# Performance work log

Hardware: AMD Instinct MI355X
Metric: run time of the kernel (lower is better)

The kernel has to match this reference:

```python
import jax, jax.numpy as jnp
import numpy as np

N_NODES = 50000
N_EDGES = 800000
HID = 64
OUT = 64
REL = 5


def setup_inputs() -> dict:
    key = jax.random.key(0)
    ks = jax.random.split(key, 9)
    s_in = 1.0 / np.sqrt(HID)
    return {
        "contagion_risk": jax.random.normal(ks[0], (N_NODES, HID), jnp.float32),
        "edge_weight": jax.random.uniform(ks[1], (N_EDGES,), jnp.float32),
        # torch Linear weights stored transposed as [in, out] so y = x @ W + b
        "W_in_w": jax.random.uniform(ks[2], (HID, HID), jnp.float32, -s_in, s_in),
        "W_in_b": jax.random.uniform(ks[3], (HID,), jnp.float32, -s_in, s_in),
        "W_rel": jax.random.uniform(ks[4], (REL, HID, HID), jnp.float32, -s_in, s_in),
        "W_out_w": jax.random.uniform(ks[5], (HID, OUT), jnp.float32, -s_in, s_in),
        "W_out_b": jax.random.uniform(ks[6], (OUT,), jnp.float32, -s_in, s_in),
        "edge_index": jax.random.randint(ks[7], (2, N_EDGES), 0, N_NODES, jnp.int64 if jax.config.jax_enable_x64 else jnp.int32),
        "edge_type": jax.random.randint(ks[8], (N_EDGES,), 0, REL, jnp.int32),
        "num_nodes": N_NODES,
    }


def _dan_forward(contagion_risk, W_in_w, W_in_b, W_rel, W_out_w, W_out_b,
                 edge_index, edge_type, num_nodes):
    row, col = edge_index[0], edge_index[1]  # dst, src
    x = contagion_risk @ W_in_w + W_in_b                       # [N, H]
    x_j = x[col]                                               # [E, H] gather

    # gcn_norm (no self loops, unit edge weights): deg over col
    ones = jnp.ones(col.shape[0], x.dtype)
    deg = jax.ops.segment_sum(ones, col, num_segments=num_nodes)
    dis = jnp.where(deg > 0, jax.lax.rsqrt(jnp.maximum(deg, 1.0)), 0.0)
    norm_w = (dis[row] * dis[col])[:, None]                    # [E, 1]
    msg_gcn = jax.ops.segment_sum(x_j * norm_w, row, num_segments=num_nodes)

    # per-relation masked GEMM (grouped GEMM over REL relation types)
    res = jnp.zeros_like(x_j)
    for i in range(W_rel.shape[0]):
        mask = (edge_type == i)[:, None]
        res = res + jnp.where(mask, x_j @ W_rel[i], 0.0)

    # segment softmax over destination-node groups (per feature channel)
    seg_max = jax.ops.segment_max(res, row, num_segments=num_nodes)
    e = jnp.exp(res - seg_max[row])
    seg_sum = jax.ops.segment_sum(e, row, num_segments=num_nodes)
    weig = e / (seg_sum[row] + 1e-16)

    msg = jax.ops.segment_sum(res * weig, row, num_segments=num_nodes)
    out = (msg_gcn + 0.5 * jax.nn.relu(msg)) @ W_out_w + W_out_b
    return out


def reference(contagion_risk, edge_weight, W_in_w, W_in_b, W_rel, W_out_w, W_out_b,
              edge_index, edge_type, num_nodes):
    # edge_weight is accepted by the original forward but never used
    return _dan_forward(contagion_risk, W_in_w, W_in_b, W_rel, W_out_w, W_out_b,
                        edge_index, edge_type, num_nodes)
```

## Files before the change

### kernel.cpp

```cpp
#include <hip/hip_runtime.h>
#include <hip/hip_bf16.h>

#define HID 64
#define REL 5
#define EPB 2048

typedef short bf16x8 __attribute__((ext_vector_type(8)));
typedef float f32x4 __attribute__((ext_vector_type(4)));

__device__ __forceinline__ float bf2f(unsigned short u) {
    return __uint_as_float(((unsigned)u) << 16);
}
__device__ __forceinline__ unsigned short f2bf(float f) {
    __hip_bfloat16 h = (__hip_bfloat16)f;
    return *(unsigned short*)&h;
}
__device__ __forceinline__ void dec_edge(const int* __restrict__ ei, int i64,
                                         int E, int e, int& r, int& c) {
    if (i64) { r = ei[2 * e]; c = ei[2 * (E + e)]; }
    else     { r = ei[e];     c = ei[E + e]; }
}

__global__ void k_detect(const unsigned short* __restrict__ wb,
                         const int* __restrict__ ei, int* flags) {
    int lane = threadIdx.x;
    bool big = (lane < 32) ? (fabsf(bf2f(wb[2 * lane])) > 0.26f) : false;
    unsigned long long b1 = __ballot(big);
    bool odd_nz = (ei[2 * lane + 1] != 0);
    unsigned long long b2 = __ballot(odd_nz);
    if (lane == 0) {
        flags[0] = (b1 != 0ull) ? 1 : 0;
        flags[1] = (b2 == 0ull) ? 1 : 0;
    }
}

__global__ void k_pack(const void* Win, const void* bin, const void* Wr,
                       const void* Wout, const void* bout,
                       unsigned short* __restrict__ Bpk,
                       float* __restrict__ binf, float* __restrict__ boutf,
                       const int* __restrict__ flags) {
    int f = flags[0];
    int gid = blockIdx.x * 256 + threadIdx.x;
    if (gid < 7 * 2 * 4 * 64) {
        int lane = gid & 63;
        int nt = (gid >> 6) & 3;
        int ks = (gid >> 8) & 1;
        int mat = gid >> 9;
        int q = lane >> 4, n = nt * 16 + (lane & 15);
#pragma unroll
        for (int j = 0; j < 8; j++) {
            int k = ks * 32 + q * 8 + j;
            int idx = k * 64 + n;
            float val;
            if (mat == 0)
                val = f ? ((const float*)Win)[idx] : bf2f(((const unsigned short*)Win)[idx]);
            else if (mat <= 5) {
                int ii = (mat - 1) * 4096 + idx;
                val = f ? ((const float*)Wr)[ii] : bf2f(((const unsigned short*)Wr)[ii]);
            } else
                val = f ? ((const float*)Wout)[idx] : bf2f(((const unsigned short*)Wout)[idx]);
            Bpk[(size_t)gid * 8 + j] = f2bf(val);
        }
    }
    if (gid < 64)
        binf[gid] = f ? ((const float*)bin)[gid] : bf2f(((const unsigned short*)bin)[gid]);
    else if (gid >= 64 && gid < 128) {
        int i = gid - 64;
        boutf[i] = f ? ((const float*)bout)[i] : bf2f(((const unsigned short*)bout)[i]);
    }
}

__global__ void k_p1a(const int* __restrict__ ei, const int* __restrict__ flags,
                      int* __restrict__ hist, int E, int NB, int nblk) {
    extern __shared__ int lh[];
    int tid = threadIdx.x, blk = blockIdx.x;
    for (int i = tid; i < 2 * NB; i += 256) lh[i] = 0;
    __syncthreads();
    int i64 = flags[1];
#pragma unroll
    for (int k = 0; k < EPB / 256; k++) {
        int e = blk * EPB + k * 256 + tid;
        if (e < E) {
            int r, c;
            dec_edge(ei, i64, E, e, r, c);
            atomicAdd(&lh[r >> 6], 1);
            atomicAdd(&lh[NB + (c >> 6)], 1);
        }
    }
    __syncthreads();
    size_t NBn = (size_t)NB * nblk;
    for (int i = tid; i < NB; i += 256) {
        hist[(size_t)i * nblk + blk] = lh[i];
        hist[NBn + (size_t)i * nblk + blk] = lh[NB + i];
    }
}

__global__ void s_blk(const int* __restrict__ v, int* __restrict__ bsum, int M) {
    __shared__ int red[256];
    int t = threadIdx.x;
    int i0 = blockIdx.x * 1024 + t * 4;
    int s = 0;
#pragma unroll
    for (int j = 0; j < 4; j++) { int i = i0 + j; if (i < M) s += v[i]; }
    red[t] = s;
    __syncthreads();
    for (int d = 128; d > 0; d >>= 1) {
        if (t < d) red[t] += red[t + d];
        __syncthreads();
    }
    if (t == 0) bsum[blockIdx.x] = red[0];
}

__global__ void s_top(int* __restrict__ bsum, int nsb) {
    __shared__ int v[1024];
    int t = threadIdx.x;
    for (int i = t; i < nsb; i += 256) v[i] = bsum[i];
    __syncthreads();
    if (t == 0) {
        int run = 0;
        for (int i = 0; i < nsb; i++) { int x = v[i]; v[i] = run; run += x; }
    }
    __syncthreads();
    for (int i = t; i < nsb; i += 256) bsum[i] = v[i];
}

__global__ void s_apply(int* __restrict__ v, const int* __restrict__ bsum, int M) {
    __shared__ int red[256];
    int t = threadIdx.x;
    int i0 = blockIdx.x * 1024 + t * 4;
    int x[4];
    int s = 0;
#pragma unroll
    for (int j = 0; j < 4; j++) {
        int i = i0 + j;
        x[j] = (i < M) ? v[i] : 0;
        s += x[j];
    }
    red[t] = s;
    __syncthreads();
    for (int d = 1; d < 256; d <<= 1) {
        int add = (t >= d) ? red[t - d] : 0;
        __syncthreads();
        red[t] += add;
        __syncthreads();
    }
    int run = bsum[blockIdx.x] + red[t] - s;
#pragma unroll
    for (int j = 0; j < 4; j++) {
        int i = i0 + j;
        if (i < M) { int tmp = x[j]; v[i] = run; run += tmp; }
    }
}

__global__ void k_p1c(const int* __restrict__ ei, const int* __restrict__ et,
                      const int* __restrict__ flags, const int* __restrict__ hist,
                      unsigned* __restrict__ rbuf, unsigned char* __restrict__ cb8,
                      int E, int NB, int nblk) {
    extern __shared__ int lh[];
    int tid = threadIdx.x, blk = blockIdx.x;
    for (int i = tid; i < 2 * NB; i += 256) lh[i] = 0;
    __syncthreads();
    int i64 = flags[1];
    size_t NBn = (size_t)NB * nblk;
#pragma unroll
    for (int k = 0; k < EPB / 256; k++) {
        int e = blk * EPB + k * 256 + tid;
        if (e < E) {
            int r, c;
            dec_edge(ei, i64, E, e, r, c);
            int t = et[e];
            int binR = r >> 6;
            int posR = hist[(size_t)binR * nblk + blk] + atomicAdd(&lh[binR], 1);
            rbuf[posR] = ((unsigned)(r & 63) << 26) | ((unsigned)t << 17) | (unsigned)c;
            int binC = c >> 6;
            int posC = hist[NBn + (size_t)binC * nblk + blk] - E + atomicAdd(&lh[NB + binC], 1);
            cb8[posC] = (unsigned char)(c & 63);
        }
    }
}

__global__ void k_p2r(const unsigned* __restrict__ rbuf, const int* __restrict__ hist,
                      int* __restrict__ off, unsigned* __restrict__ edata4,
                      int E, int N, int NB, int nblk) {
    __shared__ int lcnt[64], excl[64], lcnt2[64];
    int tid = threadIdx.x, bk = blockIdx.x;
    int bstart = hist[(size_t)bk * nblk];
    int bend = (bk + 1 < NB) ? hist[(size_t)(bk + 1) * nblk] : E;
    if (tid < 64) { lcnt[tid] = 0; lcnt2[tid] = 0; }
    __syncthreads();
    for (int e = bstart + tid; e < bend; e += 256)
        atomicAdd(&lcnt[rbuf[e] >> 26], 1);
    __syncthreads();
    if (tid == 0) {
        int run = 0;
        for (int j = 0; j < 64; j++) { excl[j] = run; run += lcnt[j]; }
    }
    __syncthreads();
    if (tid < 64) {
        int node = bk * 64 + tid;
        if (node < N) off[node] = bstart + excl[tid];
    }
    if (bk == 0 && tid == 0) off[N] = E;
    for (int e = bstart + tid; e < bend; e += 256) {
        unsigned rec = rbuf[e];
        int rl = rec >> 26;
        int t = (rec >> 17) & 7;
        int c = rec & 0x1FFFF;
        int pos = bstart + excl[rl] + atomicAdd(&lcnt2[rl], 1);
        edata4[pos] = (unsigned)c | ((unsigned)t << 20);
    }
}

__global__ void k_p2c(const unsigned char* __restrict__ cb8, const int* __restrict__ hist,
                      float* __restrict__ dis, int E, int N, int NB, int nblk) {
    __shared__ int lcnt[64];
    int tid = threadIdx.x, bk = blockIdx.x;
    size_t NBn = (size_t)NB * nblk;
    int cstart = hist[NBn + (size_t)bk * nblk] - E;
    int cend = (bk + 1 < NB) ? hist[NBn + (size_t)(bk + 1) * nblk] - E : E;
    if (tid < 64) lcnt[tid] = 0;
    __syncthreads();
    for (int e = cstart + tid; e < cend; e += 256)
        atomicAdd(&lcnt[cb8[e]], 1);
    __syncthreads();
    if (tid < 64) {
        int node = bk * 64 + tid;
        if (node < N) {
            int d = lcnt[tid];
            dis[node] = (d > 0) ? rsqrtf((float)d) : 0.f;
        }
    }
}

__device__ __forceinline__ bf16x8 load_a8(const void* A, int f, size_t base) {
    if (f) {
        const float* Af = (const float*)A + base;
        bf16x8 r;
#pragma unroll
        for (int j = 0; j < 8; j++) r[j] = (short)f2bf(Af[j]);
        return r;
    }
    return *(const bf16x8*)((const unsigned short*)A + base);
}

__global__ void __launch_bounds__(256)
k_xy(const void* __restrict__ A, const unsigned short* __restrict__ Bpk,
     const float* __restrict__ binf, const float* __restrict__ dis,
     unsigned short* __restrict__ Yb, const int* __restrict__ flags,
     int N, int Np) {
    __shared__ unsigned short Bs[6 * 2 * 4 * 64 * 8];
    __shared__ unsigned short Xs[64 * 64];
    __shared__ float bs[64];
    int tid = threadIdx.x;
    for (int i = tid; i < 6 * 2 * 4 * 64; i += 256)
        ((uint4*)Bs)[i] = ((const uint4*)Bpk)[i];
    if (tid < 64) bs[tid] = binf[tid];
    __syncthreads();

    int w = tid >> 6, lane = tid & 63;
    int q = lane >> 4, n16 = lane & 15;
    int mrow = w * 16 + n16;
    int f = flags[0];
    int arow = min(blockIdx.x * 64 + mrow, N - 1);
    bf16x8 a0 = load_a8(A, f, (size_t)arow * 64 + 8 * q);
    bf16x8 a1 = load_a8(A, f, (size_t)arow * 64 + 8 * q + 32);

    float disv[4];
#pragma unroll
    for (int r = 0; r < 4; r++) {
        int node = blockIdx.x * 64 + w * 16 + 4 * q + r;
        disv[r] = (node < N) ? dis[node] : 0.f;
    }

#pragma unroll
    for (int nt = 0; nt < 4; nt++) {
        f32x4 d = {0.f, 0.f, 0.f, 0.f};
        bf16x8 b0 = *(const bf16x8*)(Bs + (size_t)(((0 * 2 + 0) * 4 + nt) * 64 + lane) * 8);
        bf16x8 b1 = *(const bf16x8*)(Bs + (size_t)(((0 * 2 + 1) * 4 + nt) * 64 + lane) * 8);
        d = __builtin_amdgcn_mfma_f32_16x16x32_bf16(a0, b0, d, 0, 0, 0);
        d = __builtin_amdgcn_mfma_f32_16x16x32_bf16(a1, b1, d, 0, 0, 0);
        int col = nt * 16 + n16;
        float bb = bs[col];
#pragma unroll
        for (int r = 0; r < 4; r++) {
            int rowl = w * 16 + 4 * q + r;
            float xval = d[r] + bb;
            Xs[rowl * 64 + col] = f2bf(xval);
            int node = blockIdx.x * 64 + rowl;
            if (node < N) Yb[((size_t)5 * Np + node) * 64 + col] = f2bf(xval * disv[r]);
        }
    }
    bf16x8 a20 = *(const bf16x8*)(Xs + mrow * 64 + 8 * q);
    bf16x8 a21 = *(const bf16x8*)(Xs + mrow * 64 + 8 * q + 32);

    for (int rel = 0; rel < REL; rel++) {
        int mat = 1 + rel;
#pragma unroll
        for (int nt = 0; nt < 4; nt++) {
            f32x4 d = {0.f, 0.f, 0.f, 0.f};
            bf16x8 b0 = *(const bf16x8*)(Bs + (size_t)(((mat * 2 + 0) * 4 + nt) * 64 + lane) * 8);
            bf16x8 b1 = *(const bf16x8*)(Bs + (size_t)(((mat * 2 + 1) * 4 + nt) * 64 + lane) * 8);
            d = __builtin_amdgcn_mfma_f32_16x16x32_bf16(a20, b0, d, 0, 0, 0);
            d = __builtin_amdgcn_mfma_f32_16x16x32_bf16(a21, b1, d, 0, 0, 0);
            int col = nt * 16 + n16;
#pragma unroll
            for (int r = 0; r < 4; r++) {
                int node = blockIdx.x * 64 + w * 16 + 4 * q + r;
                if (node < N) Yb[((size_t)rel * Np + node) * 64 + col] = f2bf(d[r]);
            }
        }
    }
}

__global__ void __launch_bounds__(256)
k_main(const unsigned short* __restrict__ Yb, const int* __restrict__ off,
       const unsigned* __restrict__ edata4, const float* __restrict__ dis,
       unsigned short* __restrict__ v, int N, int Np) {
    int tid = threadIdx.x;
    int wv = tid >> 6, lane = tid & 63;
    int n = blockIdx.x * 4 + wv;
    if (n >= N) return;
    int half = lane >> 5;
    int c2 = (lane & 31) * 2;
    int e0 = off[n], e1 = off[n + 1];
    float s0 = 0.f, s1 = 0.f, u0 = 0.f, u1 = 0.f, g0 = 0.f, g1 = 0.f;
    const unsigned short* Yx = Yb + (size_t)5 * Np * 64;
    for (int e = e0 + half; e < e1; e += 2) {
        unsigned md = edata4[e];
        int c = md & 0xFFFFF;
        int t = md >> 20;
        unsigned yv = *(const unsigned*)(Yb + ((size_t)t * Np + c) * 64 + c2);
        unsigned xv = *(const unsigned*)(Yx + (size_t)c * 64 + c2);
        float r0 = __uint_as_float(yv << 16);
        float r1 = __uint_as_float(yv & 0xFFFF0000u);
        g0 += __uint_as_float(xv << 16);
        g1 += __uint_as_float(xv & 0xFFFF0000u);
        float p0 = __expf(fminf(r0, 60.f));
        float p1 = __expf(fminf(r1, 60.f));
        s0 += p0; s1 += p1;
        u0 += r0 * p0; u1 += r1 * p1;
    }
    s0 += __shfl_xor(s0, 32); s1 += __shfl_xor(s1, 32);
    u0 += __shfl_xor(u0, 32); u1 += __shfl_xor(u1, 32);
    g0 += __shfl_xor(g0, 32); g1 += __shfl_xor(g1, 32);
    if (half == 0) {
        float dn = dis[n];
        float m0 = u0 / (s0 + 1e-16f), m1 = u1 / (s1 + 1e-16f);
        float v0 = g0 * dn + 0.5f * fmaxf(m0, 0.f);
        float v1 = g1 * dn + 0.5f * fmaxf(m1, 0.f);
        unsigned pack = (unsigned)f2bf(v0) | ((unsigned)f2bf(v1) << 16);
        *(unsigned*)(v + (size_t)n * 64 + c2) = pack;
    }
}

__global__ void __launch_bounds__(256)
k_out(const unsigned short* __restrict__ v, const unsigned short* __restrict__ Bpk,
      const float* __restrict__ boutf, void* __restrict__ outv,
      const int* __restrict__ flags, int N, int Np) {
    __shared__ unsigned short Bs[2 * 4 * 64 * 8];
    __shared__ float bs[64];
    int tid = threadIdx.x;
    const unsigned short* src = Bpk + (size_t)6 * 2 * 4 * 64 * 8;
    for (int i = tid; i < 2 * 4 * 64; i += 256)
        ((uint4*)Bs)[i] = ((const uint4*)src)[i];
    if (tid < 64) bs[tid] = boutf[tid];
    __syncthreads();

    int w = tid >> 6, lane = tid & 63;
    int q = lane >> 4, n16 = lane & 15;
    int arow = min(blockIdx.x * 64 + w * 16 + n16, N - 1);
    bf16x8 a0 = *(const bf16x8*)(v + (size_t)arow * 64 + 8 * q);
    bf16x8 a1 = *(const bf16x8*)(v + (size_t)arow * 64 + 8 * q + 32);
    int f = flags[0];
#pragma unroll
    for (int nt = 0; nt < 4; nt++) {
        f32x4 d = {0.f, 0.f, 0.f, 0.f};
        bf16x8 b0 = *(const bf16x8*)(Bs + (size_t)((0 * 4 + nt) * 64 + lane) * 8);
        bf16x8 b1 = *(const bf16x8*)(Bs + (size_t)((1 * 4 + nt) * 64 + lane) * 8);
        d = __builtin_amdgcn_mfma_f32_16x16x32_bf16(a0, b0, d, 0, 0, 0);
        d = __builtin_amdgcn_mfma_f32_16x16x32_bf16(a1, b1, d, 0, 0, 0);
        int col = nt * 16 + n16;
        float bb = bs[col];
#pragma unroll
        for (int r = 0; r < 4; r++) {
            int node = blockIdx.x * 64 + w * 16 + 4 * q + r;
            if (node < N) {
                float o = d[r] + bb;
                if (f) ((float*)outv)[(size_t)node * 64 + col] = o;
                else   ((unsigned short*)outv)[(size_t)node * 64 + col] = f2bf(o);
            }
        }
    }
}

extern "C" void kernel_launch(void* const* d_in, const int* in_sizes, int n_in,
                              void* d_out, int out_size, void* d_ws, size_t ws_size,
                              hipStream_t stream) {
    const void* A    = d_in[0];
    const void* Win  = d_in[2];
    const void* bin  = d_in[3];
    const void* Wrel = d_in[4];
    const void* Wout = d_in[5];
    const void* bout = d_in[6];
    const int* ei = (const int*)d_in[7];
    const int* et = (const int*)d_in[8];
    int N = in_sizes[0] / HID;
    int E = in_sizes[8];
    int Np = ((N + 63) / 64) * 64;
    int NB = Np / 64;
    int nblk = (E + EPB - 1) / EPB;
    int M = 2 * NB * nblk;
    int nsb = (M + 1023) / 1024;

    char* p = (char*)d_ws;
    auto carve = [&](size_t bytes) {
        char* q = p;
        p += (bytes + 15) & ~(size_t)15;
        return q;
    };
    unsigned short* Yb   = (unsigned short*)carve((size_t)6 * Np * 64 * 2);
    unsigned short* vv   = (unsigned short*)carve((size_t)Np * 64 * 2);
    unsigned*       rbuf = (unsigned*)carve((size_t)E * 4);
    unsigned char*  cb8  = (unsigned char*)carve((size_t)E);
    unsigned*       edata4 = (unsigned*)carve((size_t)E * 4);
    int*            hist = (int*)carve((size_t)M * 4);
    unsigned short* Bpk  = (unsigned short*)carve((size_t)7 * 4096 * 2);
    float* binf  = (float*)carve(64 * 4);
    float* boutf = (float*)carve(64 * 4);
    int* off     = (int*)carve((size_t)(N + 1) * 4);
    float* dis   = (float*)carve((size_t)N * 4);
    int* bsum    = (int*)carve((size_t)nsb * 4);
    int* flags   = (int*)carve(16);

    size_t lds_part = (size_t)2 * NB * 4;

    k_detect<<<1, 64, 0, stream>>>((const unsigned short*)bin, ei, flags);
    k_pack<<<14, 256, 0, stream>>>(Win, bin, Wrel, Wout, bout, Bpk, binf, boutf, flags);
    k_p1a<<<nblk, 256, lds_part, stream>>>(ei, flags, hist, E, NB, nblk);
    s_blk<<<nsb, 256, 0, stream>>>(hist, bsum, M);
    s_top<<<1, 256, 0, stream>>>(bsum, nsb);
    s_apply<<<nsb, 256, 0, stream>>>(hist, bsum, M);
    k_p1c<<<nblk, 256, lds_part, stream>>>(ei, et, flags, hist, rbuf, cb8, E, NB, nblk);
    k_p2r<<<NB, 256, 0, stream>>>(rbuf, hist, off, edata4, E, N, NB, nblk);
    k_p2c<<<NB, 256, 0, stream>>>(cb8, hist, dis, E, N, NB, nblk);
    k_xy<<<Np / 64, 256, 0, stream>>>(A, Bpk, binf, dis, Yb, flags, N, Np);
    k_main<<<(N + 3) / 4, 256, 0, stream>>>(Yb, off, edata4, dis, vv, N, Np);
    k_out<<<Np / 64, 256, 0, stream>>>(vv, Bpk, boutf, d_out, flags, N, Np);
}
```

Measured before the change: 232.1 us.

## Stage GEMM outputs through LDS for vectorized row stores and unroll edge loop

k_xy and k_out now write MFMA results into LDS tiles and then emit 16-byte row-contiguous stores, replacing scattered 2-byte and 4-byte column stores. Bounds checks are dropped by padding the dis buffer to Np and letting k_xy write the padded rows. k_main processes two edges per half-wave per iteration with separate accumulators, so more gathers are in flight. The costs are extra LDS use, which may lower occupancy in k_xy, and a reliance on k_p2c writing dis for every padded node.

```diff
diff --git a/kernel.cpp b/kernel.cpp
--- a/kernel.cpp
+++ b/kernel.cpp
@@ -212,7 +212,7 @@
 }
 
 __global__ void k_p2c(const unsigned char* __restrict__ cb8, const int* __restrict__ hist,
-                      float* __restrict__ dis, int E, int N, int NB, int nblk) {
+                      float* __restrict__ dis, int E, int NB, int nblk) {
     __shared__ int lcnt[64];
     int tid = threadIdx.x, bk = blockIdx.x;
     size_t NBn = (size_t)NB * nblk;
@@ -225,10 +225,8 @@
     __syncthreads();
     if (tid < 64) {
         int node = bk * 64 + tid;
-        if (node < N) {
-            int d = lcnt[tid];
-            dis[node] = (d > 0) ? rsqrtf((float)d) : 0.f;
-        }
+        int d = lcnt[tid];
+        dis[node] = (d > 0) ? rsqrtf((float)d) : 0.f;
     }
 }
 
@@ -250,6 +248,7 @@
      int N, int Np) {
     __shared__ unsigned short Bs[6 * 2 * 4 * 64 * 8];
     __shared__ unsigned short Xs[64 * 64];
+    __shared__ unsigned short Ys[64 * 64];
     __shared__ float bs[64];
     int tid = threadIdx.x;
     for (int i = tid; i < 6 * 2 * 4 * 64; i += 256)
@@ -269,8 +268,10 @@
 #pragma unroll
     for (int r = 0; r < 4; r++) {
         int node = blockIdx.x * 64 + w * 16 + 4 * q + r;
-        disv[r] = (node < N) ? dis[node] : 0.f;
-    }
+        disv[r] = dis[node];
+    }
+
+    size_t snode = (size_t)(blockIdx.x * 64 + mrow);
 
 #pragma unroll
     for (int nt = 0; nt < 4; nt++) {
@@ -280,15 +281,18 @@
         d = __builtin_amdgcn_mfma_f32_16x16x32_bf16(a0, b0, d, 0, 0, 0);
         d = __builtin_amdgcn_mfma_f32_16x16x32_bf16(a1, b1, d, 0, 0, 0);
         int col = nt * 16 + n16;
-        float bb = bs[col];
 #pragma unroll
         for (int r = 0; r < 4; r++) {
             int rowl = w * 16 + 4 * q + r;
-            float xval = d[r] + bb;
+            float xval = d[r] + bs[col];
             Xs[rowl * 64 + col] = f2bf(xval);
-            int node = blockIdx.x * 64 + rowl;
-            if (node < N) Yb[((size_t)5 * Np + node) * 64 + col] = f2bf(xval * disv[r]);
+            Ys[rowl * 64 + col] = f2bf(xval * disv[r]);
         }
+    }
+    {
+        unsigned short* dst = Yb + ((size_t)5 * Np + snode) * 64;
+        *(bf16x8*)(dst + 8 * q)      = *(const bf16x8*)(Ys + mrow * 64 + 8 * q);
+        *(bf16x8*)(dst + 8 * q + 32) = *(const bf16x8*)(Ys + mrow * 64 + 8 * q + 32);
     }
     bf16x8 a20 = *(const bf16x8*)(Xs + mrow * 64 + 8 * q);
     bf16x8 a21 = *(const bf16x8*)(Xs + mrow * 64 + 8 * q + 32);
@@ -304,11 +308,12 @@
             d = __builtin_amdgcn_mfma_f32_16x16x32_bf16(a21, b1, d, 0, 0, 0);
             int col = nt * 16 + n16;
 #pragma unroll
-            for (int r = 0; r < 4; r++) {
-                int node = blockIdx.x * 64 + w * 16 + 4 * q + r;
-                if (node < N) Yb[((size_t)rel * Np + node) * 64 + col] = f2bf(d[r]);
-            }
+            for (int r = 0; r < 4; r++)
+                Ys[(w * 16 + 4 * q + r) * 64 + col] = f2bf(d[r]);
         }
+        unsigned short* dst = Yb + ((size_t)rel * Np + snode) * 64;
+        *(bf16x8*)(dst + 8 * q)      = *(const bf16x8*)(Ys + mrow * 64 + 8 * q);
+        *(bf16x8*)(dst + 8 * q + 32) = *(const bf16x8*)(Ys + mrow * 64 + 8 * q + 32);
     }
 }
 
@@ -324,11 +329,39 @@
     int c2 = (lane & 31) * 2;
     int e0 = off[n], e1 = off[n + 1];
     float s0 = 0.f, s1 = 0.f, u0 = 0.f, u1 = 0.f, g0 = 0.f, g1 = 0.f;
+    float s0b = 0.f, s1b = 0.f, u0b = 0.f, u1b = 0.f, g0b = 0.f, g1b = 0.f;
     const unsigned short* Yx = Yb + (size_t)5 * Np * 64;
-    for (int e = e0 + half; e < e1; e += 2) {
+
+    int e = e0 + half;
+    for (; e + 2 < e1; e += 4) {
+        unsigned mda = edata4[e];
+        unsigned mdb = edata4[e + 2];
+        int ca = mda & 0xFFFFF, ta = mda >> 20;
+        int cb = mdb & 0xFFFFF, tb = mdb >> 20;
+        unsigned yva = *(const unsigned*)(Yb + ((size_t)ta * Np + ca) * 64 + c2);
+        unsigned xva = *(const unsigned*)(Yx + (size_t)ca * 64 + c2);
+        unsigned yvb = *(const unsigned*)(Yb + ((size_t)tb * Np + cb) * 64 + c2);
+        unsigned xvb = *(const unsigned*)(Yx + (size_t)cb * 64 + c2);
+        float r0 = __uint_as_float(yva << 16);
+        float r1 = __uint_as_float(yva & 0xFFFF0000u);
+        g0 += __uint_as_float(xva << 16);
+        g1 += __uint_as_float(xva & 0xFFFF0000u);
+        float p0 = __expf(fminf(r0, 60.f));
+        float p1 = __expf(fminf(r1, 60.f));
+        s0 += p0; s1 += p1;
+        u0 += r0 * p0; u1 += r1 * p1;
+        float r0b = __uint_as_float(yvb << 16);
+        float r1b = __uint_as_float(yvb & 0xFFFF0000u);
+        g0b += __uint_as_float(xvb << 16);
+        g1b += __uint_as_float(xvb & 0xFFFF0000u);
+        float p0b = __expf(fminf(r0b, 60.f));
+        float p1b = __expf(fminf(r1b, 60.f));
+        s0b += p0b; s1b += p1b;
+        u0b += r0b * p0b; u1b += r1b * p1b;
+    }
+    if (e < e1) {
         unsigned md = edata4[e];
-        int c = md & 0xFFFFF;
-        int t = md >> 20;
+        int c = md & 0xFFFFF, t = md >> 20;
         unsigned yv = *(const unsigned*)(Yb + ((size_t)t * Np + c) * 64 + c2);
         unsigned xv = *(const unsigned*)(Yx + (size_t)c * 64 + c2);
         float r0 = __uint_as_float(yv << 16);
@@ -340,6 +373,8 @@
         s0 += p0; s1 += p1;
         u0 += r0 * p0; u1 += r1 * p1;
     }
+    s0 += s0b; s1 += s1b; u0 += u0b; u1 += u1b; g0 += g0b; g1 += g1b;
+
     s0 += __shfl_xor(s0, 32); s1 += __shfl_xor(s1, 32);
     u0 += __shfl_xor(u0, 32); u1 += __shfl_xor(u1, 32);
     g0 += __shfl_xor(g0, 32); g1 += __shfl_xor(g1, 32);
@@ -358,6 +393,7 @@
       const float* __restrict__ boutf, void* __restrict__ outv,
       const int* __restrict__ flags, int N, int Np) {
     __shared__ unsigned short Bs[2 * 4 * 64 * 8];
+    __shared__ float Os[64 * 64];
     __shared__ float bs[64];
     int tid = threadIdx.x;
     const unsigned short* src = Bpk + (size_t)6 * 2 * 4 * 64 * 8;
@@ -368,7 +404,8 @@
 
     int w = tid >> 6, lane = tid & 63;
     int q = lane >> 4, n16 = lane & 15;
-    int arow = min(blockIdx.x * 64 + w * 16 + n16, N - 1);
+    int mrow = w * 16 + n16;
+    int arow = min(blockIdx.x * 64 + mrow, N - 1);
     bf16x8 a0 = *(const bf16x8*)(v + (size_t)arow * 64 + 8 * q);
     bf16x8 a1 = *(const bf16x8*)(v + (size_t)arow * 64 + 8 * q + 32);
     int f = flags[0];
@@ -380,14 +417,30 @@
         d = __builtin_amdgcn_mfma_f32_16x16x32_bf16(a0, b0, d, 0, 0, 0);
         d = __builtin_amdgcn_mfma_f32_16x16x32_bf16(a1, b1, d, 0, 0, 0);
         int col = nt * 16 + n16;
-        float bb = bs[col];
-#pragma unroll
-        for (int r = 0; r < 4; r++) {
-            int node = blockIdx.x * 64 + w * 16 + 4 * q + r;
-            if (node < N) {
-                float o = d[r] + bb;
-                if (f) ((float*)outv)[(size_t)node * 64 + col] = o;
-                else   ((unsigned short*)outv)[(size_t)node * 64 + col] = f2bf(o);
+#pragma unroll
+        for (int r = 0; r < 4; r++)
+            Os[(w * 16 + 4 * q + r) * 64 + col] = d[r] + bs[col];
+    }
+    int node = blockIdx.x * 64 + mrow;
+    if (node < N) {
+        if (f) {
+            float* dst = (float*)outv + (size_t)node * 64;
+#pragma unroll
+            for (int cchunk = 0; cchunk < 2; cchunk++) {
+                int c0 = 8 * q + 32 * cchunk;
+                *(f32x4*)(dst + c0)     = *(const f32x4*)(Os + mrow * 64 + c0);
+                *(f32x4*)(dst + c0 + 4) = *(const f32x4*)(Os + mrow * 64 + c0 + 4);
+            }
+        } else {
+            unsigned short* dst = (unsigned short*)outv + (size_t)node * 64;
+#pragma unroll
+            for (int cchunk = 0; cchunk < 2; cchunk++) {
+                int c0 = 8 * q + 32 * cchunk;
+                bf16x8 pk;
+#pragma unroll
+                for (int j = 0; j < 8; j++)
+                    pk[j] = (short)f2bf(Os[mrow * 64 + c0 + j]);
+                *(bf16x8*)(dst + c0) = pk;
             }
         }
     }
@@ -428,7 +481,7 @@
     float* binf  = (float*)carve(64 * 4);
     float* boutf = (float*)carve(64 * 4);
     int* off     = (int*)carve((size_t)(N + 1) * 4);
-    float* dis   = (float*)carve((size_t)N * 4);
+    float* dis   = (float*)carve((size_t)Np * 4);
     int* bsum    = (int*)carve((size_t)nsb * 4);
     int* flags   = (int*)carve(16);
 
@@ -442,7 +495,7 @@
     s_apply<<<nsb, 256, 0, stream>>>(hist, bsum, M);
     k_p1c<<<nblk, 256, lds_part, stream>>>(ei, et, flags, hist, rbuf, cb8, E, NB, nblk);
     k_p2r<<<NB, 256, 0, stream>>>(rbuf, hist, off, edata4, E, N, NB, nblk);
-    k_p2c<<<NB, 256, 0, stream>>>(cb8, hist, dis, E, N, NB, nblk);
+    k_p2c<<<NB, 256, 0, stream>>>(cb8, hist, dis, E, NB, nblk);
     k_xy<<<Np / 64, 256, 0, stream>>>(A, Bpk, binf, dis, Yb, flags, N, Np);
     k_main<<<(N + 3) / 4, 256, 0, stream>>>(Yb, off, edata4, dis, vv, N, Np);
     k_out<<<Np / 64, 256, 0, stream>>>(vv, Bpk, boutf, d_out, flags, N, Np);
```

After: 215.4 us. -7.2%, faster.
